# Performance work log

Measured on AMD Instinct MI355X. Metric: run time of the kernel, lower is better.

Reference implementation:

```python
import jax, jax.numpy as jnp
import numpy as np

B, S, H = 2, 2048, 2048
NH, NKV, HD = 32, 8, 64
MAXP = 4096


def _apply_rope(x, cos, sin, positions):
    # x: [b, h, s, d]; cos/sin: [max_pos, d//2]; positions: [b, s]
    c = cos[positions][:, None]  # [b,1,s,d/2]
    s_ = sin[positions][:, None]
    x1 = x[..., ::2]
    x2 = x[..., 1::2]
    rotated = jnp.stack((-x2, x1), axis=-1).reshape(x.shape)  # interleave
    c2 = jnp.concatenate([c, c], axis=-1)   # repeat(1,1,1,2) tiling
    s2 = jnp.concatenate([s_, s_], axis=-1)
    return x * c2 + rotated * s2


def setup_inputs() -> dict:
    key = jax.random.key(0)
    ks = jax.random.split(key, 10)
    hidden_states = jax.random.normal(ks[0], (B, S, H), dtype=jnp.float32)
    # RoPE tables (use real rotary tables for realism)
    inv_freq = 1.0 / (10000.0 ** (jnp.arange(0, HD, 2, dtype=jnp.float32) / HD))
    t = jnp.arange(MAXP, dtype=jnp.float32)
    freqs = jnp.outer(t, inv_freq)  # [max_pos, d/2]
    cos = jnp.cos(freqs)
    sin = jnp.sin(freqs)
    positions = jnp.broadcast_to(jnp.arange(S, dtype=jnp.int32), (B, S))
    # additive causal mask
    neg = jnp.finfo(jnp.float32).min
    mask = jnp.where(jnp.tril(jnp.ones((S, S), dtype=bool)), 0.0, neg)[None, None]
    sc = 1.0 / np.sqrt(H)
    q_w = jax.random.normal(ks[1], (NH * HD, H), dtype=jnp.float32) * sc
    q_b = jnp.zeros((NH * HD,), dtype=jnp.float32)
    k_w = jax.random.normal(ks[2], (NKV * HD, H), dtype=jnp.float32) * sc
    k_b = jnp.zeros((NKV * HD,), dtype=jnp.float32)
    v_w = jax.random.normal(ks[3], (NKV * HD, H), dtype=jnp.float32) * sc
    v_b = jnp.zeros((NKV * HD,), dtype=jnp.float32)
    o_w = jax.random.normal(ks[4], (H, NH * HD), dtype=jnp.float32) * sc
    return {"hidden_states": hidden_states, "cos": cos, "sin": sin,
            "positions": positions, "mask": mask,
            "q_w": q_w, "q_b": q_b, "k_w": k_w, "k_b": k_b,
            "v_w": v_w, "v_b": v_b, "o_w": o_w}


def reference(hidden_states, cos, sin, positions, mask, q_w, q_b, k_w, k_b, v_w, v_b, o_w):
    bsz, seq_len, _ = hidden_states.shape
    groups = NH // NKV
    q = (hidden_states @ q_w.T + q_b).reshape(bsz, seq_len, NH, HD).transpose(0, 2, 1, 3)
    k = (hidden_states @ k_w.T + k_b).reshape(bsz, seq_len, NKV, HD).transpose(0, 2, 1, 3)
    v = (hidden_states @ v_w.T + v_b).reshape(bsz, seq_len, NKV, HD).transpose(0, 2, 1, 3)
    q = _apply_rope(q, cos, sin, positions)
    k = _apply_rope(k, cos, sin, positions)
    if groups > 1:
        k = jnp.repeat(k, groups, axis=1)
        v = jnp.repeat(v, groups, axis=1)
    scale = 1.0 / np.sqrt(HD)
    attn = jnp.einsum('bhqd,bhkd->bhqk', q, k) * scale
    attn = attn + mask
    attn = jax.nn.softmax(attn.astype(jnp.float32), axis=-1).astype(q.dtype)
    out = jnp.einsum('bhqk,bhkd->bhqd', attn, v)
    out = out.transpose(0, 2, 1, 3).reshape(bsz, seq_len, NH * HD)
    return out @ o_w.T
```

## Files before the change

kernel.cpp:

```cpp
#include <hip/hip_runtime.h>
#include <hip/hip_bf16.h>

#define BB   2
#define SS   2048
#define HH   2048
#define NH   32
#define NKV  8
#define HD   64
#define NTOK (BB * SS)
#define NQKV (NH * HD + 2 * NKV * HD)
#define KOFF (NH * HD)
#define VOFF (NH * HD + NKV * HD)

#define QSC  0.1803368801111244f

typedef short  short8  __attribute__((ext_vector_type(8)));
typedef short  short4v __attribute__((ext_vector_type(4)));
typedef float  float4v __attribute__((ext_vector_type(4)));

using bf16 = __hip_bfloat16;

#define DEV static __device__ __forceinline__

DEV short8 load8(const bf16* p) { return *(const short8*)p; }
DEV short8 load8s(const short* p) { return *(const short8*)p; }

DEV short f2bfbits(float f) {
    union { bf16 h; short s; } u;
    u.h = __float2bfloat16(f);
    return u.s;
}

DEV unsigned int packbf2(float a, float b) {
    return (unsigned int)(unsigned short)f2bfbits(a)
         | ((unsigned int)(unsigned short)f2bfbits(b) << 16);
}

DEV void async16(const bf16* g, short* l) {
    __builtin_amdgcn_global_load_lds(
        (const __attribute__((address_space(1))) unsigned int*)g,
        (__attribute__((address_space(3))) unsigned int*)l, 16, 0, 0);
}

__global__ __launch_bounds__(256) void cvt_all_kernel(
    const float* __restrict__ hidden, const float* __restrict__ q_w,
    const float* __restrict__ k_w, const float* __restrict__ v_w,
    const float* __restrict__ o_w,
    bf16* __restrict__ Hb, bf16* __restrict__ Wqkv, bf16* __restrict__ Wo) {
    int blk = blockIdx.x;
    const float* src;
    bf16* dst;
    int off;
    if (blk < 8192)       { src = hidden; dst = Hb;   off = blk * 1024; }
    else if (blk < 12288) { src = q_w; dst = Wqkv;    off = (blk - 8192) * 1024; }
    else if (blk < 13312) { src = k_w; dst = Wqkv + (size_t)KOFF * HH; off = (blk - 12288) * 1024; }
    else if (blk < 14336) { src = v_w; dst = Wqkv + (size_t)VOFF * HH; off = (blk - 13312) * 1024; }
    else                  { src = o_w; dst = Wo;      off = (blk - 14336) * 1024; }
    int i = off + threadIdx.x * 4;
    float4 v = *(const float4*)(src + i);
    short4v o;
    o[0] = f2bfbits(v.x); o[1] = f2bfbits(v.y);
    o[2] = f2bfbits(v.z); o[3] = f2bfbits(v.w);
    *(short4v*)(dst + i) = o;
}
#define CVT_BLOCKS 18432

struct GemmCtx {
    const bf16 *gA0, *gA1, *gB0, *gB1;
    short *lA0, *lA1, *lB0, *lB1;
    const short *rdA, *rdB;
};

DEV void gemm_setup(GemmCtx& c, const bf16* A, const bf16* Bw, int K,
                    int m0, int n0, short* As, short* Bs) {
    int lane = threadIdx.x & 63, w = threadIdx.x >> 6;
    int quad = lane >> 4, tq = lane & 15;
    int srow = lane >> 2;
    int scol = (lane & 3) * 8;
    c.gA0 = A  + (size_t)(m0 + w * 32 + srow) * K + scol;
    c.gA1 = c.gA0 + (size_t)16 * K;
    c.gB0 = Bw + (size_t)(n0 + w * 32 + srow) * K + scol;
    c.gB1 = c.gB0 + (size_t)16 * K;
    c.lA0 = As + (w * 32) * 32;
    c.lA1 = As + (w * 32 + 16) * 32;
    c.lB0 = Bs + (w * 32) * 32;
    c.lB1 = Bs + (w * 32 + 16) * 32;
    int mbase = (w >> 1) * 64, nbase = (w & 1) * 64;
    c.rdA = As + (mbase + tq) * 32 + quad * 8;
    c.rdB = Bs + (nbase + tq) * 32 + quad * 8;
}

DEV void gemm_mainloop(GemmCtx& c, int K, float4v acc[4][4]) {
    for (int k0 = 0; k0 < K; k0 += 32) {
        __syncthreads();
        async16(c.gA0 + k0, c.lA0);
        async16(c.gA1 + k0, c.lA1);
        async16(c.gB0 + k0, c.lB0);
        async16(c.gB1 + k0, c.lB1);
        __syncthreads();
        short8 af[4], bfr[4];
#pragma unroll
        for (int mi = 0; mi < 4; ++mi) af[mi]  = *(const short8*)(c.rdA + mi * 16 * 32);
#pragma unroll
        for (int nj = 0; nj < 4; ++nj) bfr[nj] = *(const short8*)(c.rdB + nj * 16 * 32);
#pragma unroll
        for (int mi = 0; mi < 4; ++mi)
#pragma unroll
            for (int nj = 0; nj < 4; ++nj)
                acc[mi][nj] = __builtin_amdgcn_mfma_f32_16x16x32_bf16(
                    af[mi], bfr[nj], acc[mi][nj], 0, 0, 0);
    }
}

__global__ __launch_bounds__(256) void qkv_kernel(
    const bf16* __restrict__ Hb, const bf16* __restrict__ Wqkv,
    const float* __restrict__ qbias, const float* __restrict__ kbias,
    const float* __restrict__ vbias,
    const float* __restrict__ cosp, const float* __restrict__ sinp,
    const int* __restrict__ posp,
    bf16* __restrict__ Qb, bf16* __restrict__ Kb, bf16* __restrict__ Vt) {
    __shared__ __align__(16) short As[128 * 32];
    __shared__ __align__(16) short Bs[128 * 32];
    int lane = threadIdx.x & 63, w = threadIdx.x >> 6;
    int quad = lane >> 4, tq = lane & 15;
    int m0 = blockIdx.y * 128, n0 = blockIdx.x * 128;
    int mbase = (w >> 1) * 64, nbase = (w & 1) * 64;

    GemmCtx c;
    gemm_setup(c, Hb, Wqkv, HH, m0, n0, As, Bs);
    float4v acc[4][4] = {};
    gemm_mainloop(c, HH, acc);

    float biasv[4];
#pragma unroll
    for (int nj = 0; nj < 4; ++nj) {
        int colg = n0 + nbase + nj * 16 + tq;
        biasv[nj] = (colg < KOFF) ? qbias[colg]
                  : (colg < VOFF) ? kbias[colg - KOFF] : vbias[colg - VOFF];
    }

#pragma unroll
    for (int mi = 0; mi < 4; ++mi) {
#pragma unroll
        for (int r = 0; r < 4; ++r) {
            int tok = m0 + mbase + mi * 16 + quad * 4 + r;
            int p = posp[tok];
#pragma unroll
            for (int nj = 0; nj < 4; ++nj) {
                int colg = n0 + nbase + nj * 16 + tq;
                float val = acc[mi][nj][r] + biasv[nj];
                if (colg < VOFF) {
                    float pv = __shfl_xor(val, 1);
                    int jh = colg & 63;
                    float Cv = cosp[p * 32 + (jh & 31)];
                    float Sv = sinp[p * 32 + (jh & 31)];
                    float outv = (jh & 1) ? (val * Cv + pv * Sv)
                                          : (val * Cv - pv * Sv);
                    if (colg < KOFF)
                        Qb[(size_t)tok * (NH * HD) + colg] = __float2bfloat16(outv * QSC);
                    else
                        Kb[(size_t)tok * (NKV * HD) + (colg - KOFF)] = __float2bfloat16(outv);
                } else {
                    int c2 = colg - VOFF;
                    int kv = c2 >> 6, d = c2 & 63;
                    int bb = tok >> 11, s = tok & (SS - 1);
                    Vt[(((size_t)bb * NKV + kv) * HD + d) * SS + s] = __float2bfloat16(val);
                }
            }
        }
    }
}

__global__ __launch_bounds__(256) void oproj_kernel(
    const bf16* __restrict__ AO, const bf16* __restrict__ Wo,
    float* __restrict__ out) {
    __shared__ __align__(16) short As[128 * 32];
    __shared__ __align__(16) short Bs[128 * 32];
    int lane = threadIdx.x & 63, w = threadIdx.x >> 6;
    int quad = lane >> 4, tq = lane & 15;
    int m0 = blockIdx.y * 128, n0 = blockIdx.x * 128;
    int mbase = (w >> 1) * 64, nbase = (w & 1) * 64;

    GemmCtx c;
    gemm_setup(c, AO, Wo, NH * HD, m0, n0, As, Bs);
    float4v acc[4][4] = {};
    gemm_mainloop(c, NH * HD, acc);

#pragma unroll
    for (int mi = 0; mi < 4; ++mi) {
#pragma unroll
        for (int nj = 0; nj < 4; ++nj) {
            int colg = n0 + nbase + nj * 16 + tq;
#pragma unroll
            for (int r = 0; r < 4; ++r) {
                int tok = m0 + mbase + mi * 16 + quad * 4 + r;
                out[(size_t)tok * HH + colg] = acc[mi][nj][r];
            }
        }
    }
}

#define PST 72

template<bool MASK>
DEV void attn_kv_step(int kv0, int qw, int w, int lane, int quad, int tq,
                      const bf16* __restrict__ Kg, const bf16* __restrict__ Vg,
                      short* Ks, short* Vs, short* myp,
                      short8 aq0, short8 aq1,
                      float4v ot[4], float& lsum) {
    int srow = lane >> 3;
    int schunk = (lane & 7) ^ (srow & 7);

    __syncthreads();
#pragma unroll
    for (int cc = 0; cc < 2; ++cc) {
        int rl = w * 16 + cc * 8;
        async16(Kg + (size_t)(kv0 + rl + srow) * (NKV * HD) + schunk * 8,
                Ks + rl * 64);
        async16(Vg + (size_t)(rl + srow) * SS + kv0 + schunk * 8,
                Vs + rl * 64);
    }
    __syncthreads();

    int p0 = (quad ^ (tq & 7)) * 8;
    float4v st[4];
#pragma unroll
    for (int t = 0; t < 4; ++t) {
        const short* kr = Ks + (t * 16 + tq) * 64;
        short8 k0 = load8s(kr + p0);
        short8 k1 = load8s(kr + (p0 ^ 32));
        float4v s = {0.f, 0.f, 0.f, 0.f};
        s = __builtin_amdgcn_mfma_f32_16x16x32_bf16(k0, aq0, s, 0, 0, 0);
        s = __builtin_amdgcn_mfma_f32_16x16x32_bf16(k1, aq1, s, 0, 0, 0);
        st[t] = s;
    }

    short8 bv[4][2];
#pragma unroll
    for (int i = 0; i < 4; ++i) {
        const short* vr = Vs + (i * 16 + tq) * 64;
        bv[i][0] = load8s(vr + p0);
        bv[i][1] = load8s(vr + (p0 ^ 32));
    }

#pragma unroll
    for (int t = 0; t < 4; ++t) {
        float p[4];
#pragma unroll
        for (int r = 0; r < 4; ++r) {
            float e = __builtin_amdgcn_exp2f(st[t][r]);
            if (MASK) {
                int kvg = kv0 + t * 16 + quad * 4 + r;
                e = (kvg <= qw) ? e : 0.f;
            }
            p[r] = e;
            lsum += e;
        }
        int pos = tq * PST + t * 16 + quad * 4;
        *(unsigned int*)(myp + pos)     = packbf2(p[0], p[1]);
        *(unsigned int*)(myp + pos + 2) = packbf2(p[2], p[3]);
    }

    short8 pf0 = load8s(myp + tq * PST + quad * 8);
    short8 pf1 = load8s(myp + tq * PST + 32 + quad * 8);

#pragma unroll
    for (int i = 0; i < 4; ++i) {
        ot[i] = __builtin_amdgcn_mfma_f32_16x16x32_bf16(bv[i][0], pf0, ot[i], 0, 0, 0);
        ot[i] = __builtin_amdgcn_mfma_f32_16x16x32_bf16(bv[i][1], pf1, ot[i], 0, 0, 0);
    }
}

DEV void attn_qblock(int qb, int b, int h, int w, int lane, int quad, int tq,
                     const bf16* __restrict__ Qb,
                     const bf16* __restrict__ Kg, const bf16* __restrict__ Vg,
                     short* Ks, short* Vs, short* myp, bf16* __restrict__ AO) {
    int q0 = qb + w * 16;
    int qw = q0 + tq;
    const bf16* Qrow = Qb + (size_t)(b * SS + q0 + tq) * (NH * HD) + h * HD + quad * 8;
    short8 aq0 = load8(Qrow);
    short8 aq1 = load8(Qrow + 32);

    float4v ot[4] = {};
    float lsum = 0.f;

    for (int kv0 = 0; kv0 < qb; kv0 += 64)
        attn_kv_step<false>(kv0, qw, w, lane, quad, tq, Kg, Vg, Ks, Vs, myp,
                            aq0, aq1, ot, lsum);
    attn_kv_step<true>(qb, qw, w, lane, quad, tq, Kg, Vg, Ks, Vs, myp,
                       aq0, aq1, ot, lsum);

    lsum += __shfl_xor(lsum, 16);
    lsum += __shfl_xor(lsum, 32);
    float inv = 1.0f / lsum;

    bf16* obase = AO + (size_t)(b * SS + q0 + tq) * (NH * HD) + h * HD + quad * 4;
#pragma unroll
    for (int i = 0; i < 4; ++i) {
        short4v o;
#pragma unroll
        for (int r = 0; r < 4; ++r) o[r] = f2bfbits(ot[i][r] * inv);
        *(short4v*)(obase + i * 16) = o;
    }
}

__global__ __launch_bounds__(256, 4) void attn_kernel(
    const bf16* __restrict__ Qb, const bf16* __restrict__ Kb,
    const bf16* __restrict__ Vt, bf16* __restrict__ AO) {
    __shared__ __align__(16) short Ks[64 * 64];
    __shared__ __align__(16) short Vs[64 * 64];
    __shared__ __align__(16) short plds[4][16 * PST];

    int lane = threadIdx.x & 63, w = threadIdx.x >> 6;
    int quad = lane >> 4, tq = lane & 15;

    int x = blockIdx.x;
    int xcd = x & 7, xi = x >> 3;
    int pair = xcd * 2 + (xi & 1);
    int b = pair >> 3, kvh = pair & 7;
    int h = kvh * 4 + (xi >> 1);

    const bf16* Kg = Kb + (size_t)(b * SS) * (NKV * HD) + kvh * HD;
    const bf16* Vg = Vt + (size_t)((b * NKV + kvh) * HD) * SS;
    short* myp = &plds[w][0];

    int jq = blockIdx.y;
    attn_qblock((31 - jq) * 64, b, h, w, lane, quad, tq, Qb, Kg, Vg, Ks, Vs, myp, AO);
    attn_qblock(jq * 64,        b, h, w, lane, quad, tq, Qb, Kg, Vg, Ks, Vs, myp, AO);
}

extern "C" void kernel_launch(void* const* d_in, const int* in_sizes, int n_in,
                              void* d_out, int out_size, void* d_ws, size_t ws_size,
                              hipStream_t stream) {
    const float* hidden = (const float*)d_in[0];
    const float* cosp   = (const float*)d_in[1];
    const float* sinp   = (const float*)d_in[2];
    const int*   posp   = (const int*)d_in[3];
    const float* q_w = (const float*)d_in[5];
    const float* q_b = (const float*)d_in[6];
    const float* k_w = (const float*)d_in[7];
    const float* k_b = (const float*)d_in[8];
    const float* v_w = (const float*)d_in[9];
    const float* v_b = (const float*)d_in[10];
    const float* o_w = (const float*)d_in[11];
    float* out = (float*)d_out;

    char* ws = (char*)d_ws;
    bf16* Hb   = (bf16*)ws; ws += (size_t)NTOK * HH * 2;
    bf16* Wqkv = (bf16*)ws; ws += (size_t)NQKV * HH * 2;
    bf16* Wo   = (bf16*)ws; ws += (size_t)HH * (NH * HD) * 2;
    bf16* Qb   = (bf16*)ws; ws += (size_t)NTOK * (NH * HD) * 2;
    bf16* Kb   = (bf16*)ws; ws += (size_t)NTOK * (NKV * HD) * 2;
    bf16* Vt   = (bf16*)ws; ws += (size_t)NTOK * (NKV * HD) * 2;
    bf16* AO   = (bf16*)ws; ws += (size_t)NTOK * (NH * HD) * 2;

    cvt_all_kernel<<<CVT_BLOCKS, 256, 0, stream>>>(
        hidden, q_w, k_w, v_w, o_w, Hb, Wqkv, Wo);

    qkv_kernel<<<dim3(NQKV / 128, NTOK / 128), 256, 0, stream>>>(
        Hb, Wqkv, q_b, k_b, v_b, cosp, sinp, posp, Qb, Kb, Vt);

    attn_kernel<<<dim3(64, 16), 256, 0, stream>>>(Qb, Kb, Vt, AO);

    oproj_kernel<<<dim3(HH / 128, NTOK / 128), 256, 0, stream>>>(AO, Wo, out);
}
```

Measured before the change: 324.0 us.

## Deepen GEMM K-tile with swizzled LDS and double attention query rows per wave

The GEMM mainloop now stages 64-wide K tiles with an XOR-swizzled LDS layout, which halves the number of barrier pairs and avoids bank conflicts. Occupancy hints are set to 3 blocks per CU. In attention, each wave now handles 32 query rows (two 16-row chunks) per superblock, so every K/V tile loaded into LDS is reused across twice as many queries. The grid is halved in y, with paired superblocks for causal load balance. In exchange, LDS use and register pressure go up, and occupancy drops to 2 blocks per CU for attention.

```diff
diff --git a/kernel.cpp b/kernel.cpp
--- a/kernel.cpp
+++ b/kernel.cpp
@@ -66,61 +66,64 @@
 #define CVT_BLOCKS 18432
 
 struct GemmCtx {
-    const bf16 *gA0, *gA1, *gB0, *gB1;
-    short *lA0, *lA1, *lB0, *lB1;
+    const bf16 *gA, *gB;
+    short *lA, *lB;
     const short *rdA, *rdB;
+    int p0;
 };
 
 DEV void gemm_setup(GemmCtx& c, const bf16* A, const bf16* Bw, int K,
                     int m0, int n0, short* As, short* Bs) {
     int lane = threadIdx.x & 63, w = threadIdx.x >> 6;
     int quad = lane >> 4, tq = lane & 15;
-    int srow = lane >> 2;
-    int scol = (lane & 3) * 8;
-    c.gA0 = A  + (size_t)(m0 + w * 32 + srow) * K + scol;
-    c.gA1 = c.gA0 + (size_t)16 * K;
-    c.gB0 = Bw + (size_t)(n0 + w * 32 + srow) * K + scol;
-    c.gB1 = c.gB0 + (size_t)16 * K;
-    c.lA0 = As + (w * 32) * 32;
-    c.lA1 = As + (w * 32 + 16) * 32;
-    c.lB0 = Bs + (w * 32) * 32;
-    c.lB1 = Bs + (w * 32 + 16) * 32;
+    int srow = lane >> 3;
+    int schunk = (lane & 7) ^ srow;
+    c.gA = A  + (size_t)(m0 + w * 32 + srow) * K + schunk * 8;
+    c.gB = Bw + (size_t)(n0 + w * 32 + srow) * K + schunk * 8;
+    c.lA = As + (w * 32) * 64;
+    c.lB = Bs + (w * 32) * 64;
     int mbase = (w >> 1) * 64, nbase = (w & 1) * 64;
-    c.rdA = As + (mbase + tq) * 32 + quad * 8;
-    c.rdB = Bs + (nbase + tq) * 32 + quad * 8;
+    c.rdA = As + (mbase + tq) * 64;
+    c.rdB = Bs + (nbase + tq) * 64;
+    c.p0 = (quad ^ (tq & 7)) * 8;
 }
 
 DEV void gemm_mainloop(GemmCtx& c, int K, float4v acc[4][4]) {
-    for (int k0 = 0; k0 < K; k0 += 32) {
+    for (int k0 = 0; k0 < K; k0 += 64) {
         __syncthreads();
-        async16(c.gA0 + k0, c.lA0);
-        async16(c.gA1 + k0, c.lA1);
-        async16(c.gB0 + k0, c.lB0);
-        async16(c.gB1 + k0, c.lB1);
+#pragma unroll
+        for (int cc = 0; cc < 4; ++cc) {
+            async16(c.gA + (size_t)cc * 8 * K + k0, c.lA + cc * 8 * 64);
+            async16(c.gB + (size_t)cc * 8 * K + k0, c.lB + cc * 8 * 64);
+        }
         __syncthreads();
-        short8 af[4], bfr[4];
-#pragma unroll
-        for (int mi = 0; mi < 4; ++mi) af[mi]  = *(const short8*)(c.rdA + mi * 16 * 32);
-#pragma unroll
-        for (int nj = 0; nj < 4; ++nj) bfr[nj] = *(const short8*)(c.rdB + nj * 16 * 32);
-#pragma unroll
-        for (int mi = 0; mi < 4; ++mi)
-#pragma unroll
-            for (int nj = 0; nj < 4; ++nj)
-                acc[mi][nj] = __builtin_amdgcn_mfma_f32_16x16x32_bf16(
-                    af[mi], bfr[nj], acc[mi][nj], 0, 0, 0);
-    }
-}
-
-__global__ __launch_bounds__(256) void qkv_kernel(
+#pragma unroll
+        for (int kh = 0; kh < 2; ++kh) {
+            int off = c.p0 ^ (kh * 32);
+            short8 af[4], bfr[4];
+#pragma unroll
+            for (int mi = 0; mi < 4; ++mi) af[mi]  = load8s(c.rdA + mi * 16 * 64 + off);
+#pragma unroll
+            for (int nj = 0; nj < 4; ++nj) bfr[nj] = load8s(c.rdB + nj * 16 * 64 + off);
+#pragma unroll
+            for (int mi = 0; mi < 4; ++mi)
+#pragma unroll
+                for (int nj = 0; nj < 4; ++nj)
+                    acc[mi][nj] = __builtin_amdgcn_mfma_f32_16x16x32_bf16(
+                        af[mi], bfr[nj], acc[mi][nj], 0, 0, 0);
+        }
+    }
+}
+
+__global__ __launch_bounds__(256, 3) void qkv_kernel(
     const bf16* __restrict__ Hb, const bf16* __restrict__ Wqkv,
     const float* __restrict__ qbias, const float* __restrict__ kbias,
     const float* __restrict__ vbias,
     const float* __restrict__ cosp, const float* __restrict__ sinp,
     const int* __restrict__ posp,
     bf16* __restrict__ Qb, bf16* __restrict__ Kb, bf16* __restrict__ Vt) {
-    __shared__ __align__(16) short As[128 * 32];
-    __shared__ __align__(16) short Bs[128 * 32];
+    __shared__ __align__(16) short As[128 * 64];
+    __shared__ __align__(16) short Bs[128 * 64];
     int lane = threadIdx.x & 63, w = threadIdx.x >> 6;
     int quad = lane >> 4, tq = lane & 15;
     int m0 = blockIdx.y * 128, n0 = blockIdx.x * 128;
@@ -171,11 +174,11 @@
     }
 }
 
-__global__ __launch_bounds__(256) void oproj_kernel(
+__global__ __launch_bounds__(256, 3) void oproj_kernel(
     const bf16* __restrict__ AO, const bf16* __restrict__ Wo,
     float* __restrict__ out) {
-    __shared__ __align__(16) short As[128 * 32];
-    __shared__ __align__(16) short Bs[128 * 32];
+    __shared__ __align__(16) short As[128 * 64];
+    __shared__ __align__(16) short Bs[128 * 64];
     int lane = threadIdx.x & 63, w = threadIdx.x >> 6;
     int quad = lane >> 4, tq = lane & 15;
     int m0 = blockIdx.y * 128, n0 = blockIdx.x * 128;
@@ -203,13 +206,12 @@
 #define PST 72
 
 template<bool MASK>
-DEV void attn_kv_step(int kv0, int qw, int w, int lane, int quad, int tq,
+DEV void attn_kv_step(int kv0, int qw0, int qw1, int w, int lane, int quad, int tq,
                       const bf16* __restrict__ Kg, const bf16* __restrict__ Vg,
                       short* Ks, short* Vs, short* myp,
-                      short8 aq0, short8 aq1,
-                      float4v ot[4], float& lsum) {
+                      const short8 (&aq)[2][2], float4v (&ot)[4][2], float (&ls)[2]) {
     int srow = lane >> 3;
-    int schunk = (lane & 7) ^ (srow & 7);
+    int schunk = (lane & 7) ^ srow;
 
     __syncthreads();
 #pragma unroll
@@ -223,93 +225,103 @@
     __syncthreads();
 
     int p0 = (quad ^ (tq & 7)) * 8;
-    float4v st[4];
+
 #pragma unroll
     for (int t = 0; t < 4; ++t) {
         const short* kr = Ks + (t * 16 + tq) * 64;
         short8 k0 = load8s(kr + p0);
         short8 k1 = load8s(kr + (p0 ^ 32));
-        float4v s = {0.f, 0.f, 0.f, 0.f};
-        s = __builtin_amdgcn_mfma_f32_16x16x32_bf16(k0, aq0, s, 0, 0, 0);
-        s = __builtin_amdgcn_mfma_f32_16x16x32_bf16(k1, aq1, s, 0, 0, 0);
-        st[t] = s;
-    }
-
-    short8 bv[4][2];
+        float4v s0 = {0.f, 0.f, 0.f, 0.f};
+        float4v s1 = {0.f, 0.f, 0.f, 0.f};
+        s0 = __builtin_amdgcn_mfma_f32_16x16x32_bf16(k0, aq[0][0], s0, 0, 0, 0);
+        s0 = __builtin_amdgcn_mfma_f32_16x16x32_bf16(k1, aq[0][1], s0, 0, 0, 0);
+        s1 = __builtin_amdgcn_mfma_f32_16x16x32_bf16(k0, aq[1][0], s1, 0, 0, 0);
+        s1 = __builtin_amdgcn_mfma_f32_16x16x32_bf16(k1, aq[1][1], s1, 0, 0, 0);
+#pragma unroll
+        for (int qc = 0; qc < 2; ++qc) {
+            const float4v& s = qc ? s1 : s0;
+            int qw = qc ? qw1 : qw0;
+            float p[4];
+#pragma unroll
+            for (int r = 0; r < 4; ++r) {
+                float e = __builtin_amdgcn_exp2f(s[r]);
+                if (MASK) {
+                    int kvg = kv0 + t * 16 + quad * 4 + r;
+                    e = (kvg <= qw) ? e : 0.f;
+                }
+                p[r] = e;
+                ls[qc] += e;
+            }
+            int pos = (qc * 16 + tq) * PST + t * 16 + quad * 4;
+            *(unsigned int*)(myp + pos)     = packbf2(p[0], p[1]);
+            *(unsigned int*)(myp + pos + 2) = packbf2(p[2], p[3]);
+        }
+    }
+
+    short8 pf00 = load8s(myp + tq * PST + quad * 8);
+    short8 pf01 = load8s(myp + tq * PST + 32 + quad * 8);
+    short8 pf10 = load8s(myp + (16 + tq) * PST + quad * 8);
+    short8 pf11 = load8s(myp + (16 + tq) * PST + 32 + quad * 8);
+
 #pragma unroll
     for (int i = 0; i < 4; ++i) {
         const short* vr = Vs + (i * 16 + tq) * 64;
-        bv[i][0] = load8s(vr + p0);
-        bv[i][1] = load8s(vr + (p0 ^ 32));
-    }
-
-#pragma unroll
-    for (int t = 0; t < 4; ++t) {
-        float p[4];
-#pragma unroll
-        for (int r = 0; r < 4; ++r) {
-            float e = __builtin_amdgcn_exp2f(st[t][r]);
-            if (MASK) {
-                int kvg = kv0 + t * 16 + quad * 4 + r;
-                e = (kvg <= qw) ? e : 0.f;
-            }
-            p[r] = e;
-            lsum += e;
-        }
-        int pos = tq * PST + t * 16 + quad * 4;
-        *(unsigned int*)(myp + pos)     = packbf2(p[0], p[1]);
-        *(unsigned int*)(myp + pos + 2) = packbf2(p[2], p[3]);
-    }
-
-    short8 pf0 = load8s(myp + tq * PST + quad * 8);
-    short8 pf1 = load8s(myp + tq * PST + 32 + quad * 8);
-
-#pragma unroll
-    for (int i = 0; i < 4; ++i) {
-        ot[i] = __builtin_amdgcn_mfma_f32_16x16x32_bf16(bv[i][0], pf0, ot[i], 0, 0, 0);
-        ot[i] = __builtin_amdgcn_mfma_f32_16x16x32_bf16(bv[i][1], pf1, ot[i], 0, 0, 0);
-    }
-}
-
-DEV void attn_qblock(int qb, int b, int h, int w, int lane, int quad, int tq,
-                     const bf16* __restrict__ Qb,
-                     const bf16* __restrict__ Kg, const bf16* __restrict__ Vg,
-                     short* Ks, short* Vs, short* myp, bf16* __restrict__ AO) {
-    int q0 = qb + w * 16;
-    int qw = q0 + tq;
-    const bf16* Qrow = Qb + (size_t)(b * SS + q0 + tq) * (NH * HD) + h * HD + quad * 8;
-    short8 aq0 = load8(Qrow);
-    short8 aq1 = load8(Qrow + 32);
-
-    float4v ot[4] = {};
-    float lsum = 0.f;
-
-    for (int kv0 = 0; kv0 < qb; kv0 += 64)
-        attn_kv_step<false>(kv0, qw, w, lane, quad, tq, Kg, Vg, Ks, Vs, myp,
-                            aq0, aq1, ot, lsum);
-    attn_kv_step<true>(qb, qw, w, lane, quad, tq, Kg, Vg, Ks, Vs, myp,
-                       aq0, aq1, ot, lsum);
-
-    lsum += __shfl_xor(lsum, 16);
-    lsum += __shfl_xor(lsum, 32);
-    float inv = 1.0f / lsum;
-
-    bf16* obase = AO + (size_t)(b * SS + q0 + tq) * (NH * HD) + h * HD + quad * 4;
-#pragma unroll
-    for (int i = 0; i < 4; ++i) {
-        short4v o;
-#pragma unroll
-        for (int r = 0; r < 4; ++r) o[r] = f2bfbits(ot[i][r] * inv);
-        *(short4v*)(obase + i * 16) = o;
-    }
-}
-
-__global__ __launch_bounds__(256, 4) void attn_kernel(
+        short8 bv0 = load8s(vr + p0);
+        short8 bv1 = load8s(vr + (p0 ^ 32));
+        ot[i][0] = __builtin_amdgcn_mfma_f32_16x16x32_bf16(bv0, pf00, ot[i][0], 0, 0, 0);
+        ot[i][0] = __builtin_amdgcn_mfma_f32_16x16x32_bf16(bv1, pf01, ot[i][0], 0, 0, 0);
+        ot[i][1] = __builtin_amdgcn_mfma_f32_16x16x32_bf16(bv0, pf10, ot[i][1], 0, 0, 0);
+        ot[i][1] = __builtin_amdgcn_mfma_f32_16x16x32_bf16(bv1, pf11, ot[i][1], 0, 0, 0);
+    }
+}
+
+DEV void attn_superblock(int sb, int b, int h, int w, int lane, int quad, int tq,
+                         const bf16* __restrict__ Qb,
+                         const bf16* __restrict__ Kg, const bf16* __restrict__ Vg,
+                         short* Ks, short* Vs, short* myp, bf16* __restrict__ AO) {
+    int qw0 = sb + w * 32 + tq;
+    int qw1 = qw0 + 16;
+    const bf16* Qr0 = Qb + (size_t)(b * SS + qw0) * (NH * HD) + h * HD + quad * 8;
+    const bf16* Qr1 = Qr0 + (size_t)16 * (NH * HD);
+    short8 aq[2][2];
+    aq[0][0] = load8(Qr0); aq[0][1] = load8(Qr0 + 32);
+    aq[1][0] = load8(Qr1); aq[1][1] = load8(Qr1 + 32);
+
+    float4v ot[4][2] = {};
+    float ls[2] = {0.f, 0.f};
+
+    for (int kv0 = 0; kv0 < sb; kv0 += 64)
+        attn_kv_step<false>(kv0, qw0, qw1, w, lane, quad, tq, Kg, Vg, Ks, Vs, myp,
+                            aq, ot, ls);
+    attn_kv_step<true>(sb, qw0, qw1, w, lane, quad, tq, Kg, Vg, Ks, Vs, myp,
+                       aq, ot, ls);
+    attn_kv_step<true>(sb + 64, qw0, qw1, w, lane, quad, tq, Kg, Vg, Ks, Vs, myp,
+                       aq, ot, ls);
+
+#pragma unroll
+    for (int qc = 0; qc < 2; ++qc) {
+        float lsum = ls[qc];
+        lsum += __shfl_xor(lsum, 16);
+        lsum += __shfl_xor(lsum, 32);
+        float inv = 1.0f / lsum;
+        int qg = qc ? qw1 : qw0;
+        bf16* obase = AO + (size_t)(b * SS + qg) * (NH * HD) + h * HD + quad * 4;
+#pragma unroll
+        for (int i = 0; i < 4; ++i) {
+            short4v o;
+#pragma unroll
+            for (int r = 0; r < 4; ++r) o[r] = f2bfbits(ot[i][qc][r] * inv);
+            *(short4v*)(obase + i * 16) = o;
+        }
+    }
+}
+
+__global__ __launch_bounds__(256, 2) void attn_kernel(
     const bf16* __restrict__ Qb, const bf16* __restrict__ Kb,
     const bf16* __restrict__ Vt, bf16* __restrict__ AO) {
     __shared__ __align__(16) short Ks[64 * 64];
     __shared__ __align__(16) short Vs[64 * 64];
-    __shared__ __align__(16) short plds[4][16 * PST];
+    __shared__ __align__(16) short plds[4][32 * PST];
 
     int lane = threadIdx.x & 63, w = threadIdx.x >> 6;
     int quad = lane >> 4, tq = lane & 15;
@@ -325,8 +337,8 @@
     short* myp = &plds[w][0];
 
     int jq = blockIdx.y;
-    attn_qblock((31 - jq) * 64, b, h, w, lane, quad, tq, Qb, Kg, Vg, Ks, Vs, myp, AO);
-    attn_qblock(jq * 64,        b, h, w, lane, quad, tq, Qb, Kg, Vg, Ks, Vs, myp, AO);
+    attn_superblock((15 - jq) * 128, b, h, w, lane, quad, tq, Qb, Kg, Vg, Ks, Vs, myp, AO);
+    attn_superblock(jq * 128,        b, h, w, lane, quad, tq, Qb, Kg, Vg, Ks, Vs, myp, AO);
 }
 
 extern "C" void kernel_launch(void* const* d_in, const int* in_sizes, int n_in,
@@ -360,7 +372,7 @@
     qkv_kernel<<<dim3(NQKV / 128, NTOK / 128), 256, 0, stream>>>(
         Hb, Wqkv, q_b, k_b, v_b, cosp, sinp, posp, Qb, Kb, Vt);
 
-    attn_kernel<<<dim3(64, 16), 256, 0, stream>>>(Qb, Kb, Vt, AO);
+    attn_kernel<<<dim3(64, 8), 256, 0, stream>>>(Qb, Kb, Vt, AO);
 
     oproj_kernel<<<dim3(HH / 128, NTOK / 128), 256, 0, stream>>>(AO, Wo, out);
 }
```

Result: faster. 296.3 us (-8.5%).
